# Optimization experiments

Hardware: AMD Instinct MI355X
Metric: run time of the kernel (lower is better)

The kernel has to match this reference:

```python
import math
import jax, jax.numpy as jnp
import numpy as np

L, E, Hn, X, K, V, B, T = 4, 512, 8, 8, 2, 32000, 8, 1024
HIGH, HID = 32000, 1024
Dh = E // Hn
HALF = Dh // 2


def _ln(x, w, b):
    m = x.mean(-1, keepdims=True)
    v = ((x - m) ** 2).mean(-1, keepdims=True)
    return (x - m) / jnp.sqrt(v + 1e-5) * w + b


def _rope_sincos(t, half):
    pos = jnp.arange(t, dtype=jnp.float32)[:, None]
    div = jnp.exp(jnp.arange(0, half * 2, 2, dtype=jnp.float32) * (-math.log(10000.0) / (half * 2)))
    ang = pos * div
    return jnp.sin(ang), jnp.cos(ang)


def setup_inputs() -> dict:
    key = jax.random.key(0)
    ks = iter(jax.random.split(key, 40))

    def nrm(shape, s=0.02):
        return jax.random.normal(next(ks), shape, dtype=jnp.float32) * s

    inp = {
        'tok_emb': nrm((V, E)), 'pos_emb': nrm((T, E)),
        'ln1_w': jnp.ones((L, E)), 'ln1_b': jnp.zeros((L, E)),
        'ln2_w': jnp.ones((L, E)), 'ln2_b': jnp.zeros((L, E)),
        'qkv_w': nrm((L, 3 * E, E)), 'out_w': nrm((L, E, E)),
        'route_w': nrm((L, X, E)), 'route_b': jnp.zeros((L, X)),
        'noise_w': nrm((L, X, E)), 'noise_b': jnp.zeros((L, X)),
        'exp_w1': nrm((L, X, 4 * E, E)), 'exp_b1': jnp.zeros((L, X, 4 * E)),
        'exp_w2': nrm((L, X, E, 4 * E)), 'exp_b2': jnp.zeros((L, X, E)),
        'lnf_w': jnp.ones(E), 'lnf_b': jnp.zeros(E),
        'pool_q': jax.random.normal(next(ks), (E,), dtype=jnp.float32),
        'pool_w': nrm((HIGH, E)), 'pool_b': jnp.zeros(HIGH),
        'head_w1': nrm((HID, HIGH)), 'head_b1': jnp.zeros(HID),
        'head_w2': nrm((1, HID)), 'head_b2': jnp.zeros(1),
        'input_ids': jax.random.randint(next(ks), (B, T), 0, V, dtype=jnp.int32),
        'router_noise': jax.random.normal(next(ks), (L, B, T, X), dtype=jnp.float32),
    }
    return inp


def _forward(tok_emb, pos_emb, ln1_w, ln1_b, ln2_w, ln2_b, qkv_w, out_w,
             route_w, route_b, noise_w, noise_b, exp_w1, exp_b1, exp_w2, exp_b2,
             lnf_w, lnf_b, pool_q, pool_w, pool_b, head_w1, head_b1, head_w2, head_b2,
             input_ids, router_noise):
    b, t = input_ids.shape
    sin, cos = _rope_sincos(t, HALF)
    sin_ = sin[None, :, None, :]
    cos_ = cos[None, :, None, :]
    cap = (b * t * K) // X  # expert_capacity, capacity_factor=1.0

    x = tok_emb[input_ids] + pos_emb[:t]
    for l in range(L):
        # --- attention (non-causal, RoPE, eval: no dropout) ---
        h = _ln(x, ln1_w[l], ln1_b[l])
        qkv = (h @ qkv_w[l].T).reshape(b, t, 3, Hn, Dh)
        q, k, v = qkv[:, :, 0], qkv[:, :, 1], qkv[:, :, 2]

        def rot(a):
            a1, a2 = a[..., :HALF], a[..., HALF:]
            return jnp.concatenate([a1 * cos_ - a2 * sin_, a2 * cos_ + a1 * sin_], axis=-1)
        q, k = rot(q), rot(k)
        scores = jnp.einsum('bthd,bshd->bhts', q, k) / math.sqrt(Dh)
        p = jax.nn.softmax(scores, axis=-1)
        att = jnp.einsum('bhts,bshd->bthd', p, v)
        # faithful to source: view(B,T,H,D).permute(0,2,1,3).reshape(B,T,C)
        att = jnp.transpose(att, (0, 2, 1, 3)).reshape(b, t, E)
        x = x + att @ out_w[l].T

        # --- noisy top-k MoE with capacity-limited dispatch ---
        h = _ln(x, ln2_w[l], ln2_b[l])
        logits = h @ route_w[l].T + route_b[l]
        nlog = h @ noise_w[l].T + noise_b[l]
        noisy = logits + router_noise[l] * jax.nn.softplus(nlog)
        topv, topi = jax.lax.top_k(noisy, K)
        pk = jax.nn.softmax(topv, axis=-1)  # softmax over sparse (-inf elsewhere)
        gate = (jax.nn.one_hot(topi, X, dtype=x.dtype) * pk[..., None]).sum(-2)  # (b,t,X)

        flat = h.reshape(-1, E)
        gflat = gate.reshape(-1, X)
        iflat = topi.reshape(-1, K)
        upd = jnp.zeros_like(flat)
        for i in range(X):
            mask = (iflat == i).any(-1)
            idx = jnp.nonzero(mask, size=cap, fill_value=0)[0]  # first `cap` selected tokens
            valid = (jnp.arange(cap) < mask.sum()).astype(x.dtype)
            tok = flat[idx]
            eo = jax.nn.relu(tok @ exp_w1[l, i].T + exp_b1[l, i]) @ exp_w2[l, i].T + exp_b2[l, i]
            g = gflat[idx, i] * valid
            upd = upd.at[idx].add(eo * g[:, None])
        x = x + upd.reshape(b, t, E)

    x = _ln(x, lnf_w, lnf_b)
    s = jnp.einsum('e,bte->bt', pool_q, x) / math.sqrt(E)
    w = jax.nn.softmax(s, axis=-1)
    pooled = jnp.einsum('bt,bte->be', w, x)
    hv = pooled @ pool_w.T + pool_b
    out = jax.nn.relu(hv @ head_w1.T + head_b1) @ head_w2.T + head_b2
    return out  # (B, 1)


def reference(tok_emb, pos_emb, ln1_w, ln1_b, ln2_w, ln2_b, qkv_w, out_w,
              route_w, route_b, noise_w, noise_b, exp_w1, exp_b1, exp_w2, exp_b2,
              lnf_w, lnf_b, pool_q, pool_w, pool_b, head_w1, head_b1, head_w2, head_b2,
              input_ids, router_noise):
    return _forward(tok_emb, pos_emb, ln1_w, ln1_b, ln2_w, ln2_b, qkv_w, out_w,
                    route_w, route_b, noise_w, noise_b, exp_w1, exp_b1, exp_w2, exp_b2,
                    lnf_w, lnf_b, pool_q, pool_w, pool_b, head_w1, head_b1, head_w2, head_b2,
                    input_ids, router_noise)
```

## Files before the change

### kernel.cpp

```cpp
#include <hip/hip_runtime.h>
#include <math.h>

constexpr int L_ = 4, E_ = 512, Hn_ = 8, X_ = 8, Kk_ = 2, V_ = 32000;
constexpr int B_ = 8, T_ = 1024, HIGH_ = 32000, HID_ = 1024;
constexpr int Dh_ = E_ / Hn_;
constexpr int HALF_ = Dh_ / 2;
constexpr int NTOK = B_ * T_;
constexpr int CAP_ = NTOK * Kk_ / X_;
constexpr int FF_ = 4 * E_;

typedef short short8 __attribute__((ext_vector_type(8)));
typedef float f32x4 __attribute__((ext_vector_type(4)));

__device__ __forceinline__ float wave_sum(float v) {
#pragma unroll
  for (int off = 32; off; off >>= 1) v += __shfl_xor(v, off, 64);
  return v;
}
__device__ __forceinline__ float wave_max(float v) {
#pragma unroll
  for (int off = 32; off; off >>= 1) v = fmaxf(v, __shfl_xor(v, off, 64));
  return v;
}

__device__ __forceinline__ unsigned short f2bf(float x) {
  union { float f; unsigned u; } v; v.f = x;
  unsigned r = v.u + 0x7FFFu + ((v.u >> 16) & 1u);
  return (unsigned short)(r >> 16);
}
__device__ __forceinline__ float bf2f(unsigned short h) {
  union { unsigned u; float f; } v; v.u = ((unsigned)h) << 16;
  return v.f;
}

__global__ __launch_bounds__(256)
void split_cast_kernel(const float* __restrict__ src, unsigned short* __restrict__ hi,
                       unsigned short* __restrict__ lo, int n) {
  int i = (blockIdx.x * 256 + threadIdx.x) * 4;
  if (i >= n) return;
  float4 v = *(const float4*)(src + i);
  float vv[4] = {v.x, v.y, v.z, v.w};
#pragma unroll
  for (int j = 0; j < 4; ++j) {
    unsigned short h = f2bf(vv[j]);
    hi[i + j] = h;
    lo[i + j] = f2bf(vv[j] - bf2f(h));
  }
}

__global__ __launch_bounds__(256)
void embed_kernel(const float* __restrict__ tok_emb, const float* __restrict__ pos_emb,
                  const int* __restrict__ ids, float* __restrict__ x) {
  int tok = blockIdx.x;
  int t = tok & (T_ - 1);
  int id = ids[tok];
  const float* te = tok_emb + (size_t)id * E_;
  const float* pe = pos_emb + (size_t)t * E_;
  float* xr = x + (size_t)tok * E_;
  int tid = threadIdx.x;
  xr[tid]       = te[tid]       + pe[tid];
  xr[tid + 256] = te[tid + 256] + pe[tid + 256];
}

__global__ __launch_bounds__(256)
void ln_kernel(const float* __restrict__ x, const float* __restrict__ w,
               const float* __restrict__ b, float* __restrict__ o) {
  int row = blockIdx.x, tid = threadIdx.x;
  const float* xr = x + (size_t)row * E_;
  float a0 = xr[tid], a1 = xr[tid + 256];
  __shared__ float red[4];
  float s = wave_sum(a0 + a1);
  if ((tid & 63) == 0) red[tid >> 6] = s;
  __syncthreads();
  float mean = (red[0] + red[1] + red[2] + red[3]) * (1.f / E_);
  float d0 = a0 - mean, d1 = a1 - mean;
  __syncthreads();
  float sq = wave_sum(d0 * d0 + d1 * d1);
  if ((tid & 63) == 0) red[tid >> 6] = sq;
  __syncthreads();
  float var = (red[0] + red[1] + red[2] + red[3]) * (1.f / E_);
  float rstd = 1.f / sqrtf(var + 1e-5f);
  float* orow = o + (size_t)row * E_;
  orow[tid]       = d0 * rstd * w[tid]       + b[tid];
  orow[tid + 256] = d1 * rstd * w[tid + 256] + b[tid + 256];
}

template <int MODE>
__global__ __launch_bounds__(256)
void mfma_gemm(const unsigned short* __restrict__ Ah, const unsigned short* __restrict__ Al,
               int lda,
               const unsigned short* __restrict__ Wh, const unsigned short* __restrict__ Wl,
               const float* __restrict__ bias, float* __restrict__ C,
               unsigned short* __restrict__ Oh, unsigned short* __restrict__ Ol,
               const int* __restrict__ elist, const float* __restrict__ egates, int e0,
               int M, int N, int K) {
  int z = blockIdx.z;
  const int* rows = nullptr;
  const float* gates = nullptr;
  if (MODE == 2) {
    Wh += (size_t)z * N * K;  Wl += (size_t)z * N * K;
    bias += (size_t)(e0 + z) * N;
    rows = elist + (size_t)(e0 + z) * CAP_;
    Oh += (size_t)z * M * N;  Ol += (size_t)z * M * N;
  }
  if (MODE == 3) {
    Ah += (size_t)z * M * K;  Al += (size_t)z * M * K;
    Wh += (size_t)z * N * K;  Wl += (size_t)z * N * K;
    bias += (size_t)(e0 + z) * N;
    rows = elist + (size_t)(e0 + z) * CAP_;
    gates = egates + (size_t)(e0 + z) * CAP_;
  }

  __shared__ __align__(16) unsigned short Ah_s[128][40];
  __shared__ __align__(16) unsigned short Al_s[128][40];
  __shared__ __align__(16) unsigned short Bh_s[128][40];
  __shared__ __align__(16) unsigned short Bl_s[128][40];

  int tid = threadIdx.x;
  int m0 = blockIdx.y * 128, n0 = blockIdx.x * 128;
  int w = tid >> 6, lane = tid & 63;
  int wm = w >> 1, wn = w & 1;
  int lm = lane & 15, q8 = (lane >> 4) * 8, q4 = (lane >> 4) * 4;

  int r = tid >> 1, seg = tid & 1;
  size_t arow = (MODE == 2) ? (size_t)rows[m0 + r] : (size_t)(m0 + r);
  const unsigned short* pAh = Ah + arow * (size_t)lda + seg * 16;
  const unsigned short* pAl = Al + arow * (size_t)lda + seg * 16;
  const unsigned short* pWh = Wh + (size_t)(n0 + r) * K + seg * 16;
  const unsigned short* pWl = Wl + (size_t)(n0 + r) * K + seg * 16;

  f32x4 acc[4][4];
#pragma unroll
  for (int i = 0; i < 4; ++i)
#pragma unroll
    for (int j = 0; j < 4; ++j) acc[i][j] = {0.f, 0.f, 0.f, 0.f};

  for (int k0 = 0; k0 < K; k0 += 32) {
    uint4 a0 = *(const uint4*)(pAh + k0);
    uint4 a1 = *(const uint4*)(pAh + k0 + 8);
    uint4 l0 = *(const uint4*)(pAl + k0);
    uint4 l1 = *(const uint4*)(pAl + k0 + 8);
    uint4 b0 = *(const uint4*)(pWh + k0);
    uint4 b1 = *(const uint4*)(pWh + k0 + 8);
    uint4 c0 = *(const uint4*)(pWl + k0);
    uint4 c1 = *(const uint4*)(pWl + k0 + 8);
    *(uint4*)&Ah_s[r][seg * 16]     = a0;
    *(uint4*)&Ah_s[r][seg * 16 + 8] = a1;
    *(uint4*)&Al_s[r][seg * 16]     = l0;
    *(uint4*)&Al_s[r][seg * 16 + 8] = l1;
    *(uint4*)&Bh_s[r][seg * 16]     = b0;
    *(uint4*)&Bh_s[r][seg * 16 + 8] = b1;
    *(uint4*)&Bl_s[r][seg * 16]     = c0;
    *(uint4*)&Bl_s[r][seg * 16 + 8] = c1;
    __syncthreads();

    short8 aH[4], aL[4], bH[4], bL[4];
#pragma unroll
    for (int i = 0; i < 4; ++i) {
      aH[i] = *(const short8*)&Ah_s[wm * 64 + i * 16 + lm][q8];
      aL[i] = *(const short8*)&Al_s[wm * 64 + i * 16 + lm][q8];
    }
#pragma unroll
    for (int j = 0; j < 4; ++j) {
      bH[j] = *(const short8*)&Bh_s[wn * 64 + j * 16 + lm][q8];
      bL[j] = *(const short8*)&Bl_s[wn * 64 + j * 16 + lm][q8];
    }
#pragma unroll
    for (int i = 0; i < 4; ++i)
#pragma unroll
      for (int j = 0; j < 4; ++j) {
        acc[i][j] = __builtin_amdgcn_mfma_f32_16x16x32_bf16(aH[i], bH[j], acc[i][j], 0, 0, 0);
        acc[i][j] = __builtin_amdgcn_mfma_f32_16x16x32_bf16(aH[i], bL[j], acc[i][j], 0, 0, 0);
        acc[i][j] = __builtin_amdgcn_mfma_f32_16x16x32_bf16(aL[i], bH[j], acc[i][j], 0, 0, 0);
      }
    __syncthreads();
  }

#pragma unroll
  for (int i = 0; i < 4; ++i) {
#pragma unroll
    for (int rg = 0; rg < 4; ++rg) {
      int m = m0 + wm * 64 + i * 16 + q4 + rg;
      int tokr = 0; float g = 0.f;
      if (MODE == 3) { tokr = rows[m]; g = gates[m]; }
#pragma unroll
      for (int j = 0; j < 4; ++j) {
        int n = n0 + wn * 64 + j * 16 + lm;
        float v = acc[i][j][rg];
        if (MODE == 0) {
          C[(size_t)m * N + n] = v;
        } else if (MODE == 1) {
          C[(size_t)m * N + n] += v;
        } else if (MODE == 2) {
          v = fmaxf(v + bias[n], 0.f);
          unsigned short hv16 = f2bf(v);
          Oh[(size_t)m * N + n] = hv16;
          Ol[(size_t)m * N + n] = f2bf(v - bf2f(hv16));
        } else {
          if (g != 0.f)
            atomicAdd(&C[(size_t)tokr * N + n], (v + bias[n]) * g);
        }
      }
    }
  }
}

__global__ __launch_bounds__(256)
void rope_kernel(float* __restrict__ qkv) {
  int tok = blockIdx.x;
  int t = tok & (T_ - 1);
  int hh = threadIdx.x >> 5, j = threadIdx.x & 31;
  float inv = __expf((float)j * (-logf(10000.f) / 32.f));
  float ang = (float)t * inv;
  float sn = sinf(ang), cs = cosf(ang);
  float* qp = qkv + (size_t)tok * 3 * E_ + hh * Dh_;
  float* kp = qp + E_;
  float q1 = qp[j], q2 = qp[j + HALF_];
  qp[j] = q1 * cs - q2 * sn;
  qp[j + HALF_] = q2 * cs + q1 * sn;
  float k1 = kp[j], k2 = kp[j + HALF_];
  kp[j] = k1 * cs - k2 * sn;
  kp[j + HALF_] = k2 * cs + k1 * sn;
}

__global__ __launch_bounds__(256)
void attn_mfma_kernel(const float* __restrict__ qkv, float* __restrict__ att) {
  __shared__ __align__(16) unsigned short Kh_s[64][72];
  __shared__ __align__(16) unsigned short Kl_s[64][72];
  __shared__ __align__(16) unsigned short Vth_s[64][72];
  __shared__ __align__(16) unsigned short Vtl_s[64][72];
  __shared__ __align__(16) unsigned short Ph_s[4][16][72];
  __shared__ __align__(16) unsigned short Pl_s[4][16][72];

  const int b = blockIdx.y >> 3, hh = blockIdx.y & 7;
  const int qt0 = blockIdx.x * 64;
  const int tid = threadIdx.x;
  const int w = tid >> 6, lane = tid & 63;
  const int lm = lane & 15, g = lane >> 4;
  const int q8 = g * 8;

  const float* base = qkv + (size_t)b * T_ * 3 * E_;

  short8 qbh[2], qbl[2];
  {
    const int t = qt0 + w * 16 + lm;
    const float* qrow = base + (size_t)t * 3 * E_ + hh * Dh_;
#pragma unroll
    for (int ks = 0; ks < 2; ++ks) {
      float4 f0 = *(const float4*)(qrow + ks * 32 + q8);
      float4 f1 = *(const float4*)(qrow + ks * 32 + q8 + 4);
      float qv[8] = {f0.x, f0.y, f0.z, f0.w, f1.x, f1.y, f1.z, f1.w};
#pragma unroll
      for (int e = 0; e < 8; ++e) {
        float sv = qv[e] * 0.125f;
        unsigned short hv = f2bf(sv);
        qbh[ks][e] = (short)hv;
        qbl[ks][e] = (short)f2bf(sv - bf2f(hv));
      }
    }
  }

  f32x4 o[4];
#pragma unroll
  for (int i = 0; i < 4; ++i) o[i] = {0.f, 0.f, 0.f, 0.f};
  float m_run = -1e30f, l_run = 0.f;

  const int r = tid >> 2, c16 = (tid & 3) * 16;

  for (int s0 = 0; s0 < T_; s0 += 64) {
    const float* krow = base + (size_t)(s0 + r) * 3 * E_ + E_ + hh * Dh_ + c16;
    const float* vrow = krow + E_;
#pragma unroll
    for (int hf = 0; hf < 2; ++hf) {
      float4 a0 = *(const float4*)(krow + hf * 8);
      float4 a1 = *(const float4*)(krow + hf * 8 + 4);
      float fa[8] = {a0.x, a0.y, a0.z, a0.w, a1.x, a1.y, a1.z, a1.w};
      unsigned short hs[8], ls[8];
#pragma unroll
      for (int j = 0; j < 8; ++j) {
        hs[j] = f2bf(fa[j]);
        ls[j] = f2bf(fa[j] - bf2f(hs[j]));
      }
      uint4 uh, ul;
      uh.x = hs[0] | ((unsigned)hs[1] << 16); uh.y = hs[2] | ((unsigned)hs[3] << 16);
      uh.z = hs[4] | ((unsigned)hs[5] << 16); uh.w = hs[6] | ((unsigned)hs[7] << 16);
      ul.x = ls[0] | ((unsigned)ls[1] << 16); ul.y = ls[2] | ((unsigned)ls[3] << 16);
      ul.z = ls[4] | ((unsigned)ls[5] << 16); ul.w = ls[6] | ((unsigned)ls[7] << 16);
      *(uint4*)&Kh_s[r][c16 + hf * 8] = uh;
      *(uint4*)&Kl_s[r][c16 + hf * 8] = ul;

      float4 c0 = *(const float4*)(vrow + hf * 8);
      float4 c1 = *(const float4*)(vrow + hf * 8 + 4);
      float fc[8] = {c0.x, c0.y, c0.z, c0.w, c1.x, c1.y, c1.z, c1.w};
#pragma unroll
      for (int j = 0; j < 8; ++j) {
        unsigned short hv = f2bf(fc[j]);
        Vth_s[c16 + hf * 8 + j][r] = hv;
        Vtl_s[c16 + hf * 8 + j][r] = f2bf(fc[j] - bf2f(hv));
      }
    }
    __syncthreads();

    f32x4 sf[4];
#pragma unroll
    for (int i = 0; i < 4; ++i) sf[i] = {0.f, 0.f, 0.f, 0.f};
#pragma unroll
    for (int ks = 0; ks < 2; ++ks) {
#pragma unroll
      for (int i = 0; i < 4; ++i) {
        short8 khf = *(const short8*)&Kh_s[i * 16 + lm][ks * 32 + q8];
        short8 klf = *(const short8*)&Kl_s[i * 16 + lm][ks * 32 + q8];
        sf[i] = __builtin_amdgcn_mfma_f32_16x16x32_bf16(khf, qbh[ks], sf[i], 0, 0, 0);
        sf[i] = __builtin_amdgcn_mfma_f32_16x16x32_bf16(klf, qbh[ks], sf[i], 0, 0, 0);
        sf[i] = __builtin_amdgcn_mfma_f32_16x16x32_bf16(khf, qbl[ks], sf[i], 0, 0, 0);
      }
    }

    float tmax = -1e30f;
#pragma unroll
    for (int i = 0; i < 4; ++i)
#pragma unroll
      for (int rg = 0; rg < 4; ++rg) tmax = fmaxf(tmax, sf[i][rg]);
    tmax = fmaxf(tmax, __shfl_xor(tmax, 16, 64));
    tmax = fmaxf(tmax, __shfl_xor(tmax, 32, 64));
    float mnew = fmaxf(m_run, tmax);
    float alpha = __expf(m_run - mnew);
    float psum = 0.f;
#pragma unroll
    for (int i = 0; i < 4; ++i)
#pragma unroll
      for (int rg = 0; rg < 4; ++rg) {
        float p = __expf(sf[i][rg] - mnew);
        sf[i][rg] = p;
        psum += p;
      }
    psum += __shfl_xor(psum, 16, 64);
    psum += __shfl_xor(psum, 32, 64);
    l_run = l_run * alpha + psum;
    m_run = mnew;
#pragma unroll
    for (int i = 0; i < 4; ++i) o[i] *= alpha;

#pragma unroll
    for (int i = 0; i < 4; ++i) {
      ushort4 ph, pl;
      float p0 = sf[i][0], p1 = sf[i][1], p2 = sf[i][2], p3 = sf[i][3];
      ph.x = f2bf(p0); pl.x = f2bf(p0 - bf2f(ph.x));
      ph.y = f2bf(p1); pl.y = f2bf(p1 - bf2f(ph.y));
      ph.z = f2bf(p2); pl.z = f2bf(p2 - bf2f(ph.z));
      ph.w = f2bf(p3); pl.w = f2bf(p3 - bf2f(ph.w));
      *(ushort4*)&Ph_s[w][lm][i * 16 + g * 4] = ph;
      *(ushort4*)&Pl_s[w][lm][i * 16 + g * 4] = pl;
    }
    asm volatile("s_waitcnt lgkmcnt(0)" ::: "memory");
    __builtin_amdgcn_sched_barrier(0);

#pragma unroll
    for (int ks = 0; ks < 2; ++ks) {
      short8 pbh = *(const short8*)&Ph_s[w][lm][ks * 32 + q8];
      short8 pbl = *(const short8*)&Pl_s[w][lm][ks * 32 + q8];
#pragma unroll
      for (int i = 0; i < 4; ++i) {
        short8 vhf = *(const short8*)&Vth_s[i * 16 + lm][ks * 32 + q8];
        short8 vlf = *(const short8*)&Vtl_s[i * 16 + lm][ks * 32 + q8];
        o[i] = __builtin_amdgcn_mfma_f32_16x16x32_bf16(vhf, pbh, o[i], 0, 0, 0);
        o[i] = __builtin_amdgcn_mfma_f32_16x16x32_bf16(vlf, pbh, o[i], 0, 0, 0);
        o[i] = __builtin_amdgcn_mfma_f32_16x16x32_bf16(vhf, pbl, o[i], 0, 0, 0);
      }
    }
    __syncthreads();
  }

  const float inv = 1.f / l_run;
  const int t = qt0 + w * 16 + lm;
  float* orow = att + ((size_t)b * T_ + hh * 128 + (t >> 3)) * E_ + (t & 7) * Dh_;
#pragma unroll
  for (int i = 0; i < 4; ++i) {
    f32x4 ov = o[i] * inv;
    *(f32x4*)(orow + i * 16 + g * 4) = ov;
  }
}

__global__ __launch_bounds__(64)
void router_kernel(const float* __restrict__ h,
                   const float* __restrict__ rw, const float* __restrict__ rb,
                   const float* __restrict__ nw, const float* __restrict__ nb,
                   const float* __restrict__ noise,
                   int* __restrict__ topi, float* __restrict__ topg) {
  int tok = blockIdx.x;
  int lane = threadIdx.x;
  const float* hr = h + (size_t)tok * E_;
  __shared__ float lg[X_], nl[X_];
  for (int xj = 0; xj < X_; ++xj) {
    float a = 0.f, c = 0.f;
    for (int dd = lane; dd < E_; dd += 64) {
      float hv = hr[dd];
      a += hv * rw[xj * E_ + dd];
      c += hv * nw[xj * E_ + dd];
    }
    a = wave_sum(a);
    c = wave_sum(c);
    if (lane == 0) { lg[xj] = a + rb[xj]; nl[xj] = c + nb[xj]; }
  }
  __syncthreads();
  if (lane == 0) {
    float noisy[X_];
#pragma unroll
    for (int xj = 0; xj < X_; ++xj) {
      float nv = nl[xj];
      float sp = fmaxf(nv, 0.f) + log1pf(expf(-fabsf(nv)));
      noisy[xj] = lg[xj] + noise[(size_t)tok * X_ + xj] * sp;
    }
    int i0 = 0;
#pragma unroll
    for (int xj = 1; xj < X_; ++xj) if (noisy[xj] > noisy[i0]) i0 = xj;
    int i1 = -1;
#pragma unroll
    for (int xj = 0; xj < X_; ++xj) {
      if (xj == i0) continue;
      if (i1 < 0 || noisy[xj] > noisy[i1]) i1 = xj;
    }
    float e = __expf(noisy[i1] - noisy[i0]);
    float p0 = 1.f / (1.f + e);
    topi[tok * 2] = i0;
    topi[tok * 2 + 1] = i1;
    topg[tok * 2] = p0;
    topg[tok * 2 + 1] = e * p0;
  }
}

__global__ __launch_bounds__(256)
void build_lists_kernel(const int* __restrict__ topi, const float* __restrict__ topg,
                        int* __restrict__ elist, float* __restrict__ eg) {
  int ex = blockIdx.x;
  int tid = threadIdx.x;
  constexpr int PER = NTOK / 256;
  int base = tid * PER;
  int cnt = 0;
  for (int i = 0; i < PER; ++i) {
    int t = base + i;
    if (topi[2 * t] == ex || topi[2 * t + 1] == ex) cnt++;
  }
  __shared__ int s[256];
  s[tid] = cnt;
  __syncthreads();
  for (int off = 1; off < 256; off <<= 1) {
    int v = (tid >= off) ? s[tid - off] : 0;
    __syncthreads();
    s[tid] += v;
    __syncthreads();
  }
  int rank = s[tid] - cnt;
  int total = s[255];
  for (int i = 0; i < PER; ++i) {
    int t = base + i;
    int k0 = topi[2 * t], k1 = topi[2 * t + 1];
    if (k0 == ex || k1 == ex) {
      if (rank < CAP_) {
        elist[ex * CAP_ + rank] = t;
        eg[ex * CAP_ + rank] = (k0 == ex) ? topg[2 * t] : topg[2 * t + 1];
      }
      rank++;
    }
  }
  for (int i = total + tid; i < CAP_; i += 256) {
    elist[ex * CAP_ + i] = 0;
    eg[ex * CAP_ + i] = 0.f;
  }
}

__global__ __launch_bounds__(64)
void pool_score_kernel(const float* __restrict__ h, const float* __restrict__ q,
                       float* __restrict__ s) {
  int tok = blockIdx.x;
  int lane = threadIdx.x;
  const float* hr = h + (size_t)tok * E_;
  float a = 0.f;
  for (int dd = lane; dd < E_; dd += 64) a += hr[dd] * q[dd];
  a = wave_sum(a);
  if (lane == 0) s[tok] = a * (1.f / sqrtf((float)E_));
}

__global__ __launch_bounds__(256)
void pool_softmax_kernel(const float* __restrict__ s, float* __restrict__ w) {
  int b = blockIdx.x, tid = threadIdx.x;
  const float* sr = s + (size_t)b * T_;
  float v[4];
  float mx = -1e30f;
#pragma unroll
  for (int i = 0; i < 4; ++i) { v[i] = sr[tid + 256 * i]; mx = fmaxf(mx, v[i]); }
  __shared__ float red[4];
  mx = wave_max(mx);
  if ((tid & 63) == 0) red[tid >> 6] = mx;
  __syncthreads();
  mx = fmaxf(fmaxf(red[0], red[1]), fmaxf(red[2], red[3]));
  float e[4], sum = 0.f;
#pragma unroll
  for (int i = 0; i < 4; ++i) { e[i] = __expf(v[i] - mx); sum += e[i]; }
  sum = wave_sum(sum);
  __syncthreads();
  if ((tid & 63) == 0) red[tid >> 6] = sum;
  __syncthreads();
  float inv = 1.f / (red[0] + red[1] + red[2] + red[3]);
#pragma unroll
  for (int i = 0; i < 4; ++i) w[(size_t)b * T_ + tid + 256 * i] = e[i] * inv;
}

__global__ __launch_bounds__(512)
void pool_weighted_kernel(const float* __restrict__ w, const float* __restrict__ h,
                          float* __restrict__ pooled) {
  int b = blockIdx.x, e = threadIdx.x;
  float acc = 0.f;
  for (int t = 0; t < T_; ++t) acc += w[(size_t)b * T_ + t] * h[((size_t)b * T_ + t) * E_ + e];
  pooled[(size_t)b * E_ + e] = acc;
}

__global__ __launch_bounds__(256)
void skinny_direct_kernel(const float* __restrict__ A, const float* __restrict__ W,
                          const float* __restrict__ bias, float* __restrict__ C, int N) {
  __shared__ float As[8 * 512];
  int tid = threadIdx.x;
  for (int i = tid; i < 8 * 512; i += 256) As[i] = A[i];
  __syncthreads();
  int wid = tid >> 6, lane = tid & 63;
  int n = blockIdx.x * 4 + wid;
  float acc[8] = {};
  const float* Wr = W + (size_t)n * 512;
#pragma unroll
  for (int it = 0; it < 2; ++it) {
    int k = it * 256 + lane * 4;
    float4 wv = *(const float4*)(Wr + k);
#pragma unroll
    for (int b = 0; b < 8; ++b) {
      float4 av = *(const float4*)(As + b * 512 + k);
      acc[b] += av.x * wv.x + av.y * wv.y + av.z * wv.z + av.w * wv.w;
    }
  }
#pragma unroll
  for (int b = 0; b < 8; ++b) {
    float s = wave_sum(acc[b]);
    if (lane == 0) C[(size_t)b * N + n] = s + bias[n];
  }
}

__global__ __launch_bounds__(256)
void init_h1_kernel(const float* __restrict__ b1, float* __restrict__ h1) {
  int idx = blockIdx.x * 256 + threadIdx.x;
  if (idx < 8 * HID_) h1[idx] = b1[idx & (HID_ - 1)];
}

__global__ __launch_bounds__(256)
void skinny_split_kernel(const float* __restrict__ A, const float* __restrict__ W,
                         float* __restrict__ C) {
  int tid = threadIdx.x;
  int wid = tid >> 6, lane = tid & 63;
  int n = blockIdx.x * 4 + wid;
  int kbase = blockIdx.y * 1280;
  const float* Wr = W + (size_t)n * HIGH_ + kbase;
  float acc[8] = {};
#pragma unroll
  for (int it = 0; it < 5; ++it) {
    int k = it * 256 + lane * 4;
    float4 wv = *(const float4*)(Wr + k);
#pragma unroll
    for (int b = 0; b < 8; ++b) {
      float4 av = *(const float4*)(A + (size_t)b * HIGH_ + kbase + k);
      acc[b] += av.x * wv.x + av.y * wv.y + av.z * wv.z + av.w * wv.w;
    }
  }
#pragma unroll
  for (int b = 0; b < 8; ++b) {
    float s = wave_sum(acc[b]);
    if (lane == 0) atomicAdd(&C[(size_t)b * HID_ + n], s);
  }
}

__global__ __launch_bounds__(256)
void head2_kernel(const float* __restrict__ h1, const float* __restrict__ w2,
                  const float* __restrict__ b2, float* __restrict__ out) {
  int b = blockIdx.x, tid = threadIdx.x;
  float a = 0.f;
  for (int j = tid; j < HID_; j += 256) a += fmaxf(h1[(size_t)b * HID_ + j], 0.f) * w2[j];
  a = wave_sum(a);
  __shared__ float red[4];
  if ((tid & 63) == 0) red[tid >> 6] = a;
  __syncthreads();
  if (tid == 0) out[b] = red[0] + red[1] + red[2] + red[3] + b2[0];
}

extern "C" void kernel_launch(void* const* d_in, const int* in_sizes, int n_in,
                              void* d_out, int out_size, void* d_ws, size_t ws_size,
                              hipStream_t stream) {
  const float* tok_emb = (const float*)d_in[0];
  const float* pos_emb = (const float*)d_in[1];
  const float* ln1_w = (const float*)d_in[2];
  const float* ln1_b = (const float*)d_in[3];
  const float* ln2_w = (const float*)d_in[4];
  const float* ln2_b = (const float*)d_in[5];
  const float* qkv_w = (const float*)d_in[6];
  const float* out_w = (const float*)d_in[7];
  const float* route_w = (const float*)d_in[8];
  const float* route_b = (const float*)d_in[9];
  const float* noise_w = (const float*)d_in[10];
  const float* noise_b = (const float*)d_in[11];
  const float* exp_w1 = (const float*)d_in[12];
  const float* exp_b1 = (const float*)d_in[13];
  const float* exp_w2 = (const float*)d_in[14];
  const float* exp_b2 = (const float*)d_in[15];
  const float* lnf_w = (const float*)d_in[16];
  const float* lnf_b = (const float*)d_in[17];
  const float* pool_q = (const float*)d_in[18];
  const float* pool_w = (const float*)d_in[19];
  const float* pool_b = (const float*)d_in[20];
  const float* head_w1 = (const float*)d_in[21];
  const float* head_b1 = (const float*)d_in[22];
  const float* head_w2 = (const float*)d_in[23];
  const float* head_b2 = (const float*)d_in[24];
  const int* ids = (const int*)d_in[25];
  const float* rnoise = (const float*)d_in[26];
  float* out = (float*)d_out;
  (void)in_sizes; (void)n_in; (void)out_size;

  constexpr size_t XE = (size_t)NTOK * E_;
  constexpr size_t W1EL = (size_t)FF_ * E_;
  constexpr size_t W2EL = (size_t)E_ * FF_;
  constexpr size_t HIDEL = (size_t)CAP_ * FF_;

  char* base = (char*)d_ws;
  size_t cur = 0;
  auto alloc_f = [&](size_t nel) { float* p = (float*)(base + cur); cur += nel * 4; return p; };
  auto alloc_u = [&](size_t nel) { unsigned short* p = (unsigned short*)(base + cur); cur += nel * 2; return p; };

  float* x = alloc_f(XE);
  float* h = alloc_f(XE);
  float* qkv = alloc_f((size_t)NTOK * 3 * E_);
  float* sbuf = alloc_f(NTOK);
  float* wbuf = alloc_f(NTOK);
  float* pooled = alloc_f(B_ * E_);
  float* hv = alloc_f((size_t)B_ * HIGH_);
  float* h1 = alloc_f(B_ * HID_);
  float* topg = alloc_f(NTOK * 2);
  float* eg = alloc_f(X_ * CAP_);
  int* topi = (int*)alloc_f(NTOK * 2);
  int* elist = (int*)alloc_f(X_ * CAP_);
  unsigned short* h2h = alloc_u(XE);
  unsigned short* h2l = alloc_u(XE);
  unsigned short* qwh = alloc_u((size_t)3 * E_ * E_);
  unsigned short* qwl = alloc_u((size_t)3 * E_ * E_);
  unsigned short* owh = alloc_u((size_t)E_ * E_);
  unsigned short* owl = alloc_u((size_t)E_ * E_);

  size_t perexp_bytes = 2ull * 2ull * (W1EL + W2EL + HIDEL);
  size_t tail_avail = (ws_size > cur) ? (ws_size - cur) : 0;
  int NB = (int)(tail_avail / perexp_bytes);
  unsigned short* earea;
  if (NB >= 1) {
    earea = (unsigned short*)(base + cur);
    if (NB > X_) NB = X_;
  } else {
    NB = 1;
    earea = (unsigned short*)qkv;
  }
  unsigned short* w1h = earea;
  unsigned short* w1l = w1h + (size_t)NB * W1EL;
  unsigned short* w2h = w1l + (size_t)NB * W1EL;
  unsigned short* w2l = w2h + (size_t)NB * W2EL;
  unsigned short* hidh = w2l + (size_t)NB * W2EL;
  unsigned short* hidl = hidh + (size_t)NB * HIDEL;

  auto cast_grid = [](size_t n) { return dim3((unsigned)((n / 4 + 255) / 256)); };

  embed_kernel<<<NTOK, 256, 0, stream>>>(tok_emb, pos_emb, ids, x);

  for (int l = 0; l < L_; ++l) {
    ln_kernel<<<NTOK, 256, 0, stream>>>(x, ln1_w + l * E_, ln1_b + l * E_, h);
    split_cast_kernel<<<cast_grid(XE), 256, 0, stream>>>(h, h2h, h2l, (int)XE);
    split_cast_kernel<<<cast_grid(3 * E_ * E_), 256, 0, stream>>>(
        qkv_w + (size_t)l * 3 * E_ * E_, qwh, qwl, 3 * E_ * E_);
    mfma_gemm<0><<<dim3(12, 64), 256, 0, stream>>>(h2h, h2l, E_, qwh, qwl, nullptr, qkv,
                                                   nullptr, nullptr, nullptr, nullptr, 0,
                                                   NTOK, 3 * E_, E_);
    rope_kernel<<<NTOK, 256, 0, stream>>>(qkv);
    {
      dim3 g(T_ / 64, B_ * Hn_);
      attn_mfma_kernel<<<g, 256, 0, stream>>>(qkv, h);
    }
    split_cast_kernel<<<cast_grid(XE), 256, 0, stream>>>(h, h2h, h2l, (int)XE);
    split_cast_kernel<<<cast_grid(E_ * E_), 256, 0, stream>>>(
        out_w + (size_t)l * E_ * E_, owh, owl, E_ * E_);
    mfma_gemm<1><<<dim3(4, 64), 256, 0, stream>>>(h2h, h2l, E_, owh, owl, nullptr, x,
                                                  nullptr, nullptr, nullptr, nullptr, 0,
                                                  NTOK, E_, E_);
    ln_kernel<<<NTOK, 256, 0, stream>>>(x, ln2_w + l * E_, ln2_b + l * E_, h);
    split_cast_kernel<<<cast_grid(XE), 256, 0, stream>>>(h, h2h, h2l, (int)XE);
    router_kernel<<<NTOK, 64, 0, stream>>>(h, route_w + (size_t)l * X_ * E_, route_b + l * X_,
                                           noise_w + (size_t)l * X_ * E_, noise_b + l * X_,
                                           rnoise + (size_t)l * NTOK * X_, topi, topg);
    build_lists_kernel<<<X_, 256, 0, stream>>>(topi, topg, elist, eg);

    for (int e0 = 0; e0 < X_; e0 += NB) {
      int nb = (X_ - e0 < NB) ? (X_ - e0) : NB;
      split_cast_kernel<<<cast_grid((size_t)nb * W1EL), 256, 0, stream>>>(
          exp_w1 + ((size_t)l * X_ + e0) * W1EL, w1h, w1l, (int)(nb * W1EL));
      split_cast_kernel<<<cast_grid((size_t)nb * W2EL), 256, 0, stream>>>(
          exp_w2 + ((size_t)l * X_ + e0) * W2EL, w2h, w2l, (int)(nb * W2EL));
      mfma_gemm<2><<<dim3(FF_ / 128, CAP_ / 128, nb), 256, 0, stream>>>(
          h2h, h2l, E_, w1h, w1l, exp_b1 + (size_t)l * X_ * FF_, nullptr,
          hidh, hidl, elist, nullptr, e0, CAP_, FF_, E_);
      mfma_gemm<3><<<dim3(E_ / 128, CAP_ / 128, nb), 256, 0, stream>>>(
          hidh, hidl, FF_, w2h, w2l, exp_b2 + (size_t)l * X_ * E_, x,
          nullptr, nullptr, elist, eg, e0, CAP_, E_, FF_);
    }
  }

  ln_kernel<<<NTOK, 256, 0, stream>>>(x, lnf_w, lnf_b, h);
  pool_score_kernel<<<NTOK, 64, 0, stream>>>(h, pool_q, sbuf);
  pool_softmax_kernel<<<B_, 256, 0, stream>>>(sbuf, wbuf);
  pool_weighted_kernel<<<B_, 512, 0, stream>>>(wbuf, h, pooled);
  skinny_direct_kernel<<<HIGH_ / 4, 256, 0, stream>>>(pooled, pool_w, pool_b, hv, HIGH_);
  init_h1_kernel<<<(8 * HID_ + 255) / 256, 256, 0, stream>>>(head_b1, h1);
  {
    dim3 g(HID_ / 4, 25);
    skinny_split_kernel<<<g, 256, 0, stream>>>(hv, head_w1, h1);
  }
  head2_kernel<<<B_, 256, 0, stream>>>(h1, head_w2, head_b2, out);
}
```

Baseline: 3.117 ms.

## Fuse bf16 split-casts into LN/attention epilogues, add split-K GEMMs and parallel pooling

LayerNorm and attention now write the hi/lo bf16 split directly, so the separate split_cast passes over the activations are gone. The out-projection and expert-down GEMMs use a split-K grid that accumulates with atomics, which doubles the number of blocks. The final pooling weighted sum is split across eight time chunks with atomic accumulation into a zeroed buffer. This removes memory round trips and raises parallelism, at the cost of extra atomic traffic and non-deterministic summation order.

```diff
diff --git a/kernel.cpp b/kernel.cpp
--- a/kernel.cpp
+++ b/kernel.cpp
@@ -62,9 +62,11 @@
   xr[tid + 256] = te[tid + 256] + pe[tid + 256];
 }
 
+template <int OUTM>
 __global__ __launch_bounds__(256)
 void ln_kernel(const float* __restrict__ x, const float* __restrict__ w,
-               const float* __restrict__ b, float* __restrict__ o) {
+               const float* __restrict__ b, float* __restrict__ o,
+               unsigned short* __restrict__ oh, unsigned short* __restrict__ ol) {
   int row = blockIdx.x, tid = threadIdx.x;
   const float* xr = x + (size_t)row * E_;
   float a0 = xr[tid], a1 = xr[tid + 256];
@@ -80,9 +82,18 @@
   __syncthreads();
   float var = (red[0] + red[1] + red[2] + red[3]) * (1.f / E_);
   float rstd = 1.f / sqrtf(var + 1e-5f);
-  float* orow = o + (size_t)row * E_;
-  orow[tid]       = d0 * rstd * w[tid]       + b[tid];
-  orow[tid + 256] = d1 * rstd * w[tid + 256] + b[tid + 256];
+  float v0 = d0 * rstd * w[tid]       + b[tid];
+  float v1 = d1 * rstd * w[tid + 256] + b[tid + 256];
+  if (OUTM & 1) {
+    float* orow = o + (size_t)row * E_;
+    orow[tid] = v0;  orow[tid + 256] = v1;
+  }
+  if (OUTM & 2) {
+    size_t base = (size_t)row * E_;
+    unsigned short h0 = f2bf(v0), h1 = f2bf(v1);
+    oh[base + tid]       = h0;  ol[base + tid]       = f2bf(v0 - bf2f(h0));
+    oh[base + tid + 256] = h1;  ol[base + tid + 256] = f2bf(v1 - bf2f(h1));
+  }
 }
 
 template <int MODE>
@@ -93,7 +104,7 @@
                const float* __restrict__ bias, float* __restrict__ C,
                unsigned short* __restrict__ Oh, unsigned short* __restrict__ Ol,
                const int* __restrict__ elist, const float* __restrict__ egates, int e0,
-               int M, int N, int K) {
+               int M, int N, int K, int n_nblk) {
   int z = blockIdx.z;
   const int* rows = nullptr;
   const float* gates = nullptr;
@@ -117,7 +128,12 @@
   __shared__ __align__(16) unsigned short Bl_s[128][40];
 
   int tid = threadIdx.x;
-  int m0 = blockIdx.y * 128, n0 = blockIdx.x * 128;
+  int nbx = blockIdx.x % n_nblk;
+  int kc  = blockIdx.x / n_nblk;
+  int KSP = gridDim.x / n_nblk;
+  int KC  = K / KSP;
+  int kbeg = kc * KC;
+  int m0 = blockIdx.y * 128, n0 = nbx * 128;
   int w = tid >> 6, lane = tid & 63;
   int wm = w >> 1, wn = w & 1;
   int lm = lane & 15, q8 = (lane >> 4) * 8, q4 = (lane >> 4) * 4;
@@ -135,7 +151,7 @@
 #pragma unroll
     for (int j = 0; j < 4; ++j) acc[i][j] = {0.f, 0.f, 0.f, 0.f};
 
-  for (int k0 = 0; k0 < K; k0 += 32) {
+  for (int k0 = kbeg; k0 < kbeg + KC; k0 += 32) {
     uint4 a0 = *(const uint4*)(pAh + k0);
     uint4 a1 = *(const uint4*)(pAh + k0 + 8);
     uint4 l0 = *(const uint4*)(pAl + k0);
@@ -190,15 +206,16 @@
         if (MODE == 0) {
           C[(size_t)m * N + n] = v;
         } else if (MODE == 1) {
-          C[(size_t)m * N + n] += v;
+          atomicAdd(&C[(size_t)m * N + n], v);
         } else if (MODE == 2) {
           v = fmaxf(v + bias[n], 0.f);
           unsigned short hv16 = f2bf(v);
           Oh[(size_t)m * N + n] = hv16;
           Ol[(size_t)m * N + n] = f2bf(v - bf2f(hv16));
         } else {
+          float bb = (kc == 0) ? bias[n] : 0.f;
           if (g != 0.f)
-            atomicAdd(&C[(size_t)tokr * N + n], (v + bias[n]) * g);
+            atomicAdd(&C[(size_t)tokr * N + n], (v + bb) * g);
         }
       }
     }
@@ -224,7 +241,8 @@
 }
 
 __global__ __launch_bounds__(256)
-void attn_mfma_kernel(const float* __restrict__ qkv, float* __restrict__ att) {
+void attn_mfma_kernel(const float* __restrict__ qkv,
+                      unsigned short* __restrict__ ohi, unsigned short* __restrict__ olo) {
   __shared__ __align__(16) unsigned short Kh_s[64][72];
   __shared__ __align__(16) unsigned short Kl_s[64][72];
   __shared__ __align__(16) unsigned short Vth_s[64][72];
@@ -373,11 +391,17 @@
 
   const float inv = 1.f / l_run;
   const int t = qt0 + w * 16 + lm;
-  float* orow = att + ((size_t)b * T_ + hh * 128 + (t >> 3)) * E_ + (t & 7) * Dh_;
+  size_t flat = ((size_t)b * T_ + hh * 128 + (t >> 3)) * E_ + (t & 7) * Dh_;
 #pragma unroll
   for (int i = 0; i < 4; ++i) {
     f32x4 ov = o[i] * inv;
-    *(f32x4*)(orow + i * 16 + g * 4) = ov;
+    ushort4 vh, vl;
+    vh.x = f2bf(ov[0]); vl.x = f2bf(ov[0] - bf2f(vh.x));
+    vh.y = f2bf(ov[1]); vl.y = f2bf(ov[1] - bf2f(vh.y));
+    vh.z = f2bf(ov[2]); vl.z = f2bf(ov[2] - bf2f(vh.z));
+    vh.w = f2bf(ov[3]); vl.w = f2bf(ov[3] - bf2f(vh.w));
+    *(ushort4*)&ohi[flat + i * 16 + g * 4] = vh;
+    *(ushort4*)&olo[flat + i * 16 + g * 4] = vl;
   }
 }
 
@@ -506,13 +530,21 @@
   for (int i = 0; i < 4; ++i) w[(size_t)b * T_ + tid + 256 * i] = e[i] * inv;
 }
 
+__global__ __launch_bounds__(256)
+void zero_kernel(float* __restrict__ p, int n) {
+  int i = blockIdx.x * 256 + threadIdx.x;
+  if (i < n) p[i] = 0.f;
+}
+
 __global__ __launch_bounds__(512)
 void pool_weighted_kernel(const float* __restrict__ w, const float* __restrict__ h,
                           float* __restrict__ pooled) {
-  int b = blockIdx.x, e = threadIdx.x;
+  int b = blockIdx.x, chunk = blockIdx.y, e = threadIdx.x;
+  int t0 = chunk * 128;
   float acc = 0.f;
-  for (int t = 0; t < T_; ++t) acc += w[(size_t)b * T_ + t] * h[((size_t)b * T_ + t) * E_ + e];
-  pooled[(size_t)b * E_ + e] = acc;
+  for (int t = t0; t < t0 + 128; ++t)
+    acc += w[(size_t)b * T_ + t] * h[((size_t)b * T_ + t) * E_ + e];
+  atomicAdd(&pooled[(size_t)b * E_ + e], acc);
 }
 
 __global__ __launch_bounds__(256)
@@ -673,26 +705,24 @@
   embed_kernel<<<NTOK, 256, 0, stream>>>(tok_emb, pos_emb, ids, x);
 
   for (int l = 0; l < L_; ++l) {
-    ln_kernel<<<NTOK, 256, 0, stream>>>(x, ln1_w + l * E_, ln1_b + l * E_, h);
-    split_cast_kernel<<<cast_grid(XE), 256, 0, stream>>>(h, h2h, h2l, (int)XE);
+    ln_kernel<2><<<NTOK, 256, 0, stream>>>(x, ln1_w + l * E_, ln1_b + l * E_,
+                                           nullptr, h2h, h2l);
     split_cast_kernel<<<cast_grid(3 * E_ * E_), 256, 0, stream>>>(
         qkv_w + (size_t)l * 3 * E_ * E_, qwh, qwl, 3 * E_ * E_);
     mfma_gemm<0><<<dim3(12, 64), 256, 0, stream>>>(h2h, h2l, E_, qwh, qwl, nullptr, qkv,
                                                    nullptr, nullptr, nullptr, nullptr, 0,
-                                                   NTOK, 3 * E_, E_);
+                                                   NTOK, 3 * E_, E_, 12);
     rope_kernel<<<NTOK, 256, 0, stream>>>(qkv);
     {
       dim3 g(T_ / 64, B_ * Hn_);
-      attn_mfma_kernel<<<g, 256, 0, stream>>>(qkv, h);
-    }
-    split_cast_kernel<<<cast_grid(XE), 256, 0, stream>>>(h, h2h, h2l, (int)XE);
+      attn_mfma_kernel<<<g, 256, 0, stream>>>(qkv, h2h, h2l);
+    }
     split_cast_kernel<<<cast_grid(E_ * E_), 256, 0, stream>>>(
         out_w + (size_t)l * E_ * E_, owh, owl, E_ * E_);
-    mfma_gemm<1><<<dim3(4, 64), 256, 0, stream>>>(h2h, h2l, E_, owh, owl, nullptr, x,
+    mfma_gemm<1><<<dim3(8, 64), 256, 0, stream>>>(h2h, h2l, E_, owh, owl, nullptr, x,
                                                   nullptr, nullptr, nullptr, nullptr, 0,
-                                                  NTOK, E_, E_);
-    ln_kernel<<<NTOK, 256, 0, stream>>>(x, ln2_w + l * E_, ln2_b + l * E_, h);
-    split_cast_kernel<<<cast_grid(XE), 256, 0, stream>>>(h, h2h, h2l, (int)XE);
+                                                  NTOK, E_, E_, 4);
+    ln_kernel<3><<<NTOK, 256, 0, stream>>>(x, ln2_w + l * E_, ln2_b + l * E_, h, h2h, h2l);
     router_kernel<<<NTOK, 64, 0, stream>>>(h, route_w + (size_t)l * X_ * E_, route_b + l * X_,
                                            noise_w + (size_t)l * X_ * E_, noise_b + l * X_,
                                            rnoise + (size_t)l * NTOK * X_, topi, topg);
@@ -706,17 +736,21 @@
           exp_w2 + ((size_t)l * X_ + e0) * W2EL, w2h, w2l, (int)(nb * W2EL));
       mfma_gemm<2><<<dim3(FF_ / 128, CAP_ / 128, nb), 256, 0, stream>>>(
           h2h, h2l, E_, w1h, w1l, exp_b1 + (size_t)l * X_ * FF_, nullptr,
-          hidh, hidl, elist, nullptr, e0, CAP_, FF_, E_);
-      mfma_gemm<3><<<dim3(E_ / 128, CAP_ / 128, nb), 256, 0, stream>>>(
+          hidh, hidl, elist, nullptr, e0, CAP_, FF_, E_, FF_ / 128);
+      mfma_gemm<3><<<dim3(E_ / 128 * 2, CAP_ / 128, nb), 256, 0, stream>>>(
           hidh, hidl, FF_, w2h, w2l, exp_b2 + (size_t)l * X_ * E_, x,
-          nullptr, nullptr, elist, eg, e0, CAP_, E_, FF_);
-    }
-  }
-
-  ln_kernel<<<NTOK, 256, 0, stream>>>(x, lnf_w, lnf_b, h);
+          nullptr, nullptr, elist, eg, e0, CAP_, E_, FF_, E_ / 128);
+    }
+  }
+
+  ln_kernel<1><<<NTOK, 256, 0, stream>>>(x, lnf_w, lnf_b, h, nullptr, nullptr);
   pool_score_kernel<<<NTOK, 64, 0, stream>>>(h, pool_q, sbuf);
   pool_softmax_kernel<<<B_, 256, 0, stream>>>(sbuf, wbuf);
-  pool_weighted_kernel<<<B_, 512, 0, stream>>>(wbuf, h, pooled);
+  zero_kernel<<<(B_ * E_ + 255) / 256, 256, 0, stream>>>(pooled, B_ * E_);
+  {
+    dim3 g(B_, 8);
+    pool_weighted_kernel<<<g, 512, 0, stream>>>(wbuf, h, pooled);
+  }
   skinny_direct_kernel<<<HIGH_ / 4, 256, 0, stream>>>(pooled, pool_w, pool_b, hv, HIGH_);
   init_h1_kernel<<<(8 * HID_ + 255) / 256, 256, 0, stream>>>(head_b1, h1);
   {
```

After: 3.224 ms. 1.03x slower.
